# Optimization experiments

Hardware: AMD Instinct MI355X
Metric: run time of the kernel (lower is better)

Reference implementation:

```python
import jax, jax.numpy as jnp
import numpy as np

B, C, H, W = 16, 3, 224, 224
P = 16
D = 768
DFF = 3072
NH = 12
HD = D // NH
L = 12
NCLS = 1000
S = (H // P) * (W // P) + 1  # 197
EPS = 1e-6


def layernorm(x, g, b):
    mu = jnp.mean(x, axis=-1, keepdims=True)
    var = jnp.mean(jnp.square(x - mu), axis=-1, keepdims=True)
    return (x - mu) * jax.lax.rsqrt(var + EPS) * g + b


def setup_inputs() -> dict:
    key = jax.random.key(0)
    ks = jax.random.split(key, 24)
    s = 0.02
    inp = {
        "x": jax.random.normal(ks[0], (B, C, H, W), jnp.float32),
        "Wconv": jax.random.normal(ks[1], (D, C, P, P), jnp.float32) * s,
        "bconv": jnp.zeros((D,), jnp.float32),
        "cls_emb": jax.random.normal(ks[2], (1, 1, D), jnp.float32) * s,
        "pos_emb": jax.random.normal(ks[3], (1, S, D), jnp.float32) * s,
        "Wq": jax.random.normal(ks[4], (L, D, D), jnp.float32) * s,
        "bq": jnp.zeros((L, D), jnp.float32),
        "Wk": jax.random.normal(ks[5], (L, D, D), jnp.float32) * s,
        "bk": jnp.zeros((L, D), jnp.float32),
        "Wv": jax.random.normal(ks[6], (L, D, D), jnp.float32) * s,
        "bv": jnp.zeros((L, D), jnp.float32),
        "Wo": jax.random.normal(ks[7], (L, D, D), jnp.float32) * s,
        "bo": jnp.zeros((L, D), jnp.float32),
        "ln1_g": jnp.ones((L, D), jnp.float32),
        "ln1_b": jnp.zeros((L, D), jnp.float32),
        "Wff1": jax.random.normal(ks[8], (L, DFF, D), jnp.float32) * s,
        "bff1": jnp.zeros((L, DFF), jnp.float32),
        "Wff2": jax.random.normal(ks[9], (L, D, DFF), jnp.float32) * s,
        "bff2": jnp.zeros((L, D), jnp.float32),
        "ln2_g": jnp.ones((L, D), jnp.float32),
        "ln2_b": jnp.zeros((L, D), jnp.float32),
        "lnf_g": jnp.ones((D,), jnp.float32),
        "lnf_b": jnp.zeros((D,), jnp.float32),
        "Whead": jax.random.normal(ks[10], (NCLS, D), jnp.float32) * s,
        "bhead": jnp.zeros((NCLS,), jnp.float32),
    }
    return inp


def reference(x, Wconv, bconv, cls_emb, pos_emb, Wq, bq, Wk, bk, Wv, bv, Wo, bo,
              ln1_g, ln1_b, Wff1, bff1, Wff2, bff2, ln2_g, ln2_b,
              lnf_g, lnf_b, Whead, bhead):
    b = x.shape[0]
    # conv patch embedding: [B, D, H/P, W/P]
    h = jax.lax.conv_general_dilated(x, Wconv, window_strides=(P, P), padding='VALID',
                                     dimension_numbers=('NCHW', 'OIHW', 'NCHW'))
    h = h + bconv[None, :, None, None]
    h = h.reshape(b, D, -1).transpose(0, 2, 1)  # [B, 196, D]
    h = jnp.concatenate([jnp.broadcast_to(cls_emb, (b, 1, D)), h], axis=1)  # [B, S, D]
    h = h + pos_emb

    scale = 1.0 / np.sqrt(HD)
    all_scores = []
    for i in range(L):
        # pre-norm MHA
        n = layernorm(h, ln1_g[i], ln1_b[i])
        q = (jnp.einsum('bsd,ed->bse', n, Wq[i]) + bq[i]).reshape(b, S, NH, HD).transpose(0, 2, 1, 3)
        k = (jnp.einsum('bsd,ed->bse', n, Wk[i]) + bk[i]).reshape(b, S, NH, HD).transpose(0, 2, 1, 3)
        v = (jnp.einsum('bsd,ed->bse', n, Wv[i]) + bv[i]).reshape(b, S, NH, HD).transpose(0, 2, 1, 3)
        scores = jax.nn.softmax(jnp.einsum('bhqd,bhkd->bhqk', q, k) * scale, axis=-1)
        attn = jnp.einsum('bhqk,bhkd->bhqd', scores, v).transpose(0, 2, 1, 3).reshape(b, S, D)
        h = h + jnp.einsum('bsd,ed->bse', attn, Wo[i]) + bo[i]
        # pre-norm FFN (exact GELU, matching torch F.gelu default)
        n = layernorm(h, ln2_g[i], ln2_b[i])
        ff = jax.nn.gelu(jnp.einsum('bsd,fd->bsf', n, Wff1[i]) + bff1[i], approximate=False)
        h = h + jnp.einsum('bsf,df->bsd', ff, Wff2[i]) + bff2[i]
        all_scores.append(scores)

    cls = layernorm(h, lnf_g, lnf_b)[:, 0]  # [B, D]
    logits = cls @ Whead.T + bhead  # [B, NCLS]
    return logits, jnp.stack(all_scores)  # scores: [L, B, NH, S, S]
```

## Files before the change

### kernel.cpp

```cpp
#include <hip/hip_runtime.h>
#include <hip/hip_bf16.h>

#define L_   12
#define B_   16
#define S_   197
#define D_   768
#define DFF_ 3072
#define NH_  12
#define HD_  64
#define NCLS_ 1000
#define MROWS (B_*S_)
#define MPAD  3200
#define SPAD  224
#define BH_   (B_*NH_)
#define SP_   232

typedef short s16x8 __attribute__((ext_vector_type(8)));
typedef float f32x4 __attribute__((ext_vector_type(4)));
typedef unsigned short u16x4 __attribute__((ext_vector_type(4)));

__device__ inline unsigned short f2b(float f) {
  unsigned u = __builtin_bit_cast(unsigned, f);
  u += 0x7fffu + ((u >> 16) & 1u);
  return (unsigned short)(u >> 16);
}

__device__ inline f32x4 mfma16(s16x8 a, s16x8 b, f32x4 c) {
  return __builtin_amdgcn_mfma_f32_16x16x32_bf16(a, b, c, 0, 0, 0);
}

__device__ inline void gload16(const void* g, void* l) {
  __builtin_amdgcn_global_load_lds(
      (const __attribute__((address_space(1))) unsigned int*)g,
      (__attribute__((address_space(3))) unsigned int*)l,
      16, 0, 0);
}

__global__ __launch_bounds__(256) void cvt_bf16(const float* __restrict__ in,
                                                unsigned short* __restrict__ out, long n4) {
  long i = (long)blockIdx.x * 256 + threadIdx.x;
  long stride = (long)gridDim.x * 256;
  for (; i < n4; i += stride) {
    f32x4 v = ((const f32x4*)in)[i];
    u16x4 o = { f2b(v[0]), f2b(v[1]), f2b(v[2]), f2b(v[3]) };
    ((u16x4*)out)[i] = o;
  }
}

__global__ __launch_bounds__(256) void cvt_qkv(const float* __restrict__ Wq,
                                               const float* __restrict__ Wk,
                                               const float* __restrict__ Wv,
                                               unsigned short* __restrict__ dst) {
  const int l = blockIdx.z, sel = blockIdx.y;
  const float* src = (sel == 0 ? Wq : (sel == 1 ? Wk : Wv)) + (size_t)l * D_ * D_;
  unsigned short* d = dst + ((size_t)l * 3 + sel) * D_ * D_;
  int i4 = blockIdx.x * 256 + threadIdx.x;
  f32x4 v = ((const f32x4*)src)[i4];
  u16x4 o = { f2b(v[0]), f2b(v[1]), f2b(v[2]), f2b(v[3]) };
  ((u16x4*)d)[i4] = o;
}

__global__ __launch_bounds__(256) void cvt_bias_qkv(const float* __restrict__ bq,
                                                    const float* __restrict__ bk,
                                                    const float* __restrict__ bv,
                                                    float* __restrict__ dst) {
  int i = blockIdx.x * 256 + threadIdx.x;
  int l = i / 2304, r = i - l * 2304;
  int sel = r / 768, c = r - sel * 768;
  dst[i] = (sel == 0 ? bq : (sel == 1 ? bk : bv))[l * 768 + c];
}

__global__ __launch_bounds__(256) void im2col(const float* __restrict__ x,
                                              unsigned short* __restrict__ Xp) {
  int idx = blockIdx.x * 256 + threadIdx.x;
  if (idx >= 3136 * 768) return;
  int m = idx / 768, kk = idx - m * 768;
  int b = m / 196, p = m - b * 196;
  int ph = p / 14, pw = p - ph * 14;
  int c = kk >> 8, rr = kk & 255;
  int i = rr >> 4, j = rr & 15;
  float v = x[(((size_t)b * 3 + c) * 224 + ph * 16 + i) * 224 + pw * 16 + j];
  Xp[idx] = f2b(v);
}

__global__ __launch_bounds__(256) void cls_init(float* __restrict__ h,
                                                const float* __restrict__ cls,
                                                const float* __restrict__ pos) {
  int idx = blockIdx.x * 256 + threadIdx.x;
  if (idx >= B_ * D_) return;
  int b = idx / D_, d = idx - b * D_;
  h[(size_t)(b * S_) * D_ + d] = cls[d] + pos[d];
}

__global__ __launch_bounds__(256) void zero_vtpad(unsigned short* __restrict__ vT) {
  int idx = blockIdx.x * 256 + threadIdx.x;
  const int n = B_ * D_ * (SPAD - S_);
  if (idx >= n) return;
  int be = idx / (SPAD - S_), s = idx - be * (SPAD - S_);
  vT[(size_t)be * SPAD + S_ + s] = 0;
}

template<int MODE, int KSPLIT>
__global__ __launch_bounds__(256) void gemm_bt(const unsigned short* __restrict__ A,
                                               const unsigned short* __restrict__ W,
                                               const float* __restrict__ bias,
                                               const float* __restrict__ pos,
                                               float* __restrict__ Cf,
                                               unsigned short* __restrict__ Cb,
                                               unsigned short* __restrict__ Cb2,
                                               unsigned short* __restrict__ Cb3,
                                               int M, int N, int K, int lda) {
  __shared__ unsigned short As[2][128 * 32];
  __shared__ unsigned short Bs[2][128 * 32];
  const int t = threadIdx.x;
  const int lane = t & 63;
  const int w = t >> 6;
  const int wr = (w >> 1) << 6;
  const int wc = (w & 1) << 6;
  const size_t tileM = (size_t)blockIdx.x * 128;
  const int tileN = blockIdx.y * 128;
  const int kbeg = (KSPLIT > 1) ? blockIdx.z * (K / KSPLIT) : 0;
  const int nsteps = (K / KSPLIT) / 32;
  const int rrow = lane & 15;
  const int kk8 = (lane >> 4) << 3;
  const int r0 = t >> 2;
  const int c0 = (t & 3) << 3;
  const unsigned short* ga0 = A + (tileM + r0) * (size_t)lda + kbeg + c0;
  const unsigned short* ga1 = ga0 + (size_t)64 * lda;
  const unsigned short* gb0 = W + ((size_t)tileN + r0) * K + kbeg + c0;
  const unsigned short* gb1 = gb0 + (size_t)64 * K;
  auto stage = [&](int buf, int kof) {
    gload16(ga0 + kof, As[buf] + w * 512);
    gload16(ga1 + kof, As[buf] + 2048 + w * 512);
    gload16(gb0 + kof, Bs[buf] + w * 512);
    gload16(gb1 + kof, Bs[buf] + 2048 + w * 512);
  };
  f32x4 acc[4][4] = {};
  stage(0, 0);
  __syncthreads();
  int cur = 0;
  for (int ks = 0; ks < nsteps; ++ks) {
    if (ks + 1 < nsteps) stage(cur ^ 1, (ks + 1) * 32);
    s16x8 af[4], bfr[4];
#pragma unroll
    for (int i = 0; i < 4; ++i)
      af[i] = *(const s16x8*)(As[cur] + (wr + i * 16 + rrow) * 32 + kk8);
#pragma unroll
    for (int i = 0; i < 4; ++i)
      bfr[i] = *(const s16x8*)(Bs[cur] + (wc + i * 16 + rrow) * 32 + kk8);
#pragma unroll
    for (int mi = 0; mi < 4; ++mi)
#pragma unroll
      for (int ni = 0; ni < 4; ++ni)
        acc[mi][ni] = mfma16(af[mi], bfr[ni], acc[mi][ni]);
    if (ks + 1 < nsteps) { __syncthreads(); cur ^= 1; }
  }
  const int rg = lane >> 4;
#pragma unroll
  for (int mi = 0; mi < 4; ++mi) {
#pragma unroll
    for (int ni = 0; ni < 4; ++ni) {
#pragma unroll
      for (int r = 0; r < 4; ++r) {
        int row = (int)tileM + wr + mi * 16 + rg * 4 + r;
        int col = tileN + wc + ni * 16 + rrow;
        if (row < M) {
          float v = acc[mi][ni][r];
          if (MODE == 2) {
            v += bias[col];
            float g = 0.5f * v * (1.0f + erff(v * 0.70710678118654752f));
            Cb[(size_t)row * N + col] = f2b(g);
          } else if (MODE == 3) {
            int bb = row / 196, pp = row - bb * 196;
            v += bias[col] + pos[(size_t)(1 + pp) * D_ + col];
            Cf[((size_t)(bb * 197 + 1 + pp)) * D_ + col] = v;
          } else if (MODE == 5) {
            v += bias[col];
            unsigned short bv = f2b(v);
            if (col < 768) {
              Cb[(size_t)row * 768 + col] = bv;
            } else if (col < 1536) {
              Cb2[(size_t)row * 768 + (col - 768)] = bv;
            } else {
              int bb = row / 197, ss = row - bb * 197;
              Cb3[((size_t)bb * D_ + (col - 1536)) * SPAD + ss] = bv;
            }
          } else if (MODE == 6) {
            Cf[((size_t)blockIdx.z * MROWS + row) * N + col] = v;
          }
        }
      }
    }
  }
}

template<int NS, bool CLS>
__global__ __launch_bounds__(256) void reduce_ln(const float* __restrict__ P,
                                                 const float* __restrict__ bias,
                                                 float* __restrict__ h,
                                                 const float* __restrict__ g,
                                                 const float* __restrict__ bb,
                                                 unsigned short* __restrict__ nbuf,
                                                 const float* __restrict__ g2,
                                                 const float* __restrict__ b2,
                                                 float* __restrict__ cls_out) {
  const int r = blockIdx.x;
  const int t = threadIdx.x;
  float* hr = h + (size_t)r * D_;
  float v[3];
#pragma unroll
  for (int j = 0; j < 3; ++j) {
    const int c = t + j * 256;
    float a = hr[c] + bias[c];
#pragma unroll
    for (int z = 0; z < NS; ++z)
      a += P[((size_t)z * MROWS + r) * D_ + c];
    v[j] = a;
  }
  float s = v[0] + v[1] + v[2];
  float s2 = v[0] * v[0] + v[1] * v[1] + v[2] * v[2];
  __shared__ float rs_[4], rs2_[4];
  const int lane = t & 63, w = t >> 6;
#pragma unroll
  for (int m = 32; m; m >>= 1) { s += __shfl_xor(s, m); s2 += __shfl_xor(s2, m); }
  if (lane == 0) { rs_[w] = s; rs2_[w] = s2; }
  __syncthreads();
  s = rs_[0] + rs_[1] + rs_[2] + rs_[3];
  s2 = rs2_[0] + rs2_[1] + rs2_[2] + rs2_[3];
  const float mu = s * (1.0f / 768.0f);
  const float var = s2 * (1.0f / 768.0f) - mu * mu;
  const float rstd = rsqrtf(var + 1e-6f);
  if (!CLS) {
    unsigned short* o = nbuf + (size_t)r * D_;
#pragma unroll
    for (int j = 0; j < 3; ++j) {
      const int c = t + j * 256;
      hr[c] = v[j];
      o[c] = f2b((v[j] - mu) * rstd * g[c] + bb[c]);
    }
  } else {
    if (r % S_ == 0) {
      float* o = cls_out + (size_t)(r / S_) * D_;
#pragma unroll
      for (int j = 0; j < 3; ++j) {
        const int c = t + j * 256;
        o[c] = (v[j] - mu) * rstd * g2[c] + b2[c];
      }
    }
  }
}

__global__ __launch_bounds__(256) void ln_rows_bf16(const float* __restrict__ x,
                                                    const float* __restrict__ g,
                                                    const float* __restrict__ bb,
                                                    unsigned short* __restrict__ out) {
  const int row = blockIdx.x;
  const float* xr = x + (size_t)row * D_;
  const int t = threadIdx.x;
  float v0 = xr[t], v1 = xr[t + 256], v2 = xr[t + 512];
  float s = v0 + v1 + v2;
  float s2 = v0 * v0 + v1 * v1 + v2 * v2;
  __shared__ float rs_[4], rs2_[4];
  const int lane = t & 63, w = t >> 6;
#pragma unroll
  for (int m = 32; m; m >>= 1) { s += __shfl_xor(s, m); s2 += __shfl_xor(s2, m); }
  if (lane == 0) { rs_[w] = s; rs2_[w] = s2; }
  __syncthreads();
  s = rs_[0] + rs_[1] + rs_[2] + rs_[3];
  s2 = rs2_[0] + rs2_[1] + rs2_[2] + rs2_[3];
  const float mu = s * (1.0f / 768.0f);
  const float var = s2 * (1.0f / 768.0f) - mu * mu;
  const float rstd = rsqrtf(var + 1e-6f);
  unsigned short* o = out + (size_t)row * D_;
  o[t]       = f2b((v0 - mu) * rstd * g[t]       + bb[t]);
  o[t + 256] = f2b((v1 - mu) * rstd * g[t + 256] + bb[t + 256]);
  o[t + 512] = f2b((v2 - mu) * rstd * g[t + 512] + bb[t + 512]);
}

__global__ __launch_bounds__(64) void attn_fused(const unsigned short* __restrict__ q,
                                                 const unsigned short* __restrict__ k,
                                                 const unsigned short* __restrict__ vT,
                                                 float* __restrict__ sout,
                                                 unsigned short* __restrict__ attn) {
  __shared__ unsigned short sP[16 * SP_];
  const int bh = blockIdx.x;
  const int b = bh / NH_, h = bh % NH_;
  const int strip = blockIdx.y;
  const int lane = threadIdx.x;
  const int rrow = lane & 15;
  const int kk8 = (lane >> 4) << 3;
  const int rg = lane >> 4;
  const unsigned short* qb = q + ((size_t)b * S_) * D_ + h * HD_;
  const unsigned short* kb = k + ((size_t)b * S_) * D_ + h * HD_;
  f32x4 acc[13] = {};
#pragma unroll
  for (int ks = 0; ks < 2; ++ks) {
    s16x8 af = *(const s16x8*)(qb + (size_t)(strip * 16 + rrow) * D_ + ks * 32 + kk8);
#pragma unroll
    for (int nf = 0; nf < 13; ++nf) {
      s16x8 bfr = *(const s16x8*)(kb + (size_t)(nf * 16 + rrow) * D_ + ks * 32 + kk8);
      acc[nf] = mfma16(af, bfr, acc[nf]);
    }
  }
#pragma unroll
  for (int r = 0; r < 4; ++r) {
    const int lr = rg * 4 + r;
    const int row = strip * 16 + lr;
    float mx = -1e30f;
#pragma unroll
    for (int nf = 0; nf < 13; ++nf) {
      int col = nf * 16 + rrow;
      float v = acc[nf][r] * 0.125f;
      if (col < S_) mx = fmaxf(mx, v);
    }
#pragma unroll
    for (int m = 1; m < 16; m <<= 1) mx = fmaxf(mx, __shfl_xor(mx, m));
    float e[13], sum = 0.f;
#pragma unroll
    for (int nf = 0; nf < 13; ++nf) {
      int col = nf * 16 + rrow;
      e[nf] = (col < S_) ? expf(acc[nf][r] * 0.125f - mx) : 0.f;
      sum += e[nf];
    }
#pragma unroll
    for (int m = 1; m < 16; m <<= 1) sum += __shfl_xor(sum, m);
    const float inv = 1.0f / sum;
    float* so = sout + ((size_t)bh * S_ + row) * S_;
#pragma unroll
    for (int nf = 0; nf < 13; ++nf) {
      int col = nf * 16 + rrow;
      float p = e[nf] * inv;
      if (row < S_ && col < S_) so[col] = p;
      sP[lr * SP_ + col] = f2b((col < S_) ? p : 0.f);
    }
  }
#pragma unroll
  for (int j = 0; j < 6; ++j) {
    int idx = lane + j * 64;
    int pr = idx / 24, pc = idx - pr * 24;
    sP[pr * SP_ + 208 + pc] = 0;
  }
  const unsigned short* Vb = vT + ((size_t)b * D_ + h * HD_) * SPAD;
  f32x4 oacc[4] = {};
#pragma unroll
  for (int ks = 0; ks < 7; ++ks) {
    s16x8 af = *(const s16x8*)(sP + rrow * SP_ + ks * 32 + kk8);
#pragma unroll
    for (int nf = 0; nf < 4; ++nf) {
      s16x8 bfr = *(const s16x8*)(Vb + (size_t)(nf * 16 + rrow) * SPAD + ks * 32 + kk8);
      oacc[nf] = mfma16(af, bfr, oacc[nf]);
    }
  }
#pragma unroll
  for (int r = 0; r < 4; ++r) {
    int row = strip * 16 + rg * 4 + r;
    if (row < S_) {
#pragma unroll
      for (int nf = 0; nf < 4; ++nf) {
        int col = h * HD_ + nf * 16 + rrow;
        attn[(size_t)(b * S_ + row) * D_ + col] = f2b(oacc[nf][r]);
      }
    }
  }
}

__global__ __launch_bounds__(256) void head_kernel(const float* __restrict__ cls_ln,
                                                   const float* __restrict__ Wh,
                                                   const float* __restrict__ bh_,
                                                   float* __restrict__ out) {
  int gw = (blockIdx.x * 256 + threadIdx.x) >> 6;
  int lane = threadIdx.x & 63;
  if (gw >= B_ * NCLS_) return;
  int b = gw / NCLS_, c = gw - b * NCLS_;
  const float* x = cls_ln + (size_t)b * D_;
  const float* wr = Wh + (size_t)c * D_;
  float s = 0.f;
  for (int d = lane; d < D_; d += 64) s += x[d] * wr[d];
#pragma unroll
  for (int m = 32; m; m >>= 1) s += __shfl_xor(s, m);
  if (lane == 0) out[(size_t)b * NCLS_ + c] = s + bh_[c];
}

extern "C" void kernel_launch(void* const* d_in, const int* in_sizes, int n_in,
                              void* d_out, int out_size, void* d_ws, size_t ws_size,
                              hipStream_t stream) {
  const float* x     = (const float*)d_in[0];
  const float* Wconv = (const float*)d_in[1];
  const float* bconv = (const float*)d_in[2];
  const float* cls_e = (const float*)d_in[3];
  const float* pos_e = (const float*)d_in[4];
  const float* Wq    = (const float*)d_in[5];
  const float* bq    = (const float*)d_in[6];
  const float* Wk    = (const float*)d_in[7];
  const float* bk    = (const float*)d_in[8];
  const float* Wv    = (const float*)d_in[9];
  const float* bv    = (const float*)d_in[10];
  const float* Wo    = (const float*)d_in[11];
  const float* bo    = (const float*)d_in[12];
  const float* ln1g  = (const float*)d_in[13];
  const float* ln1b  = (const float*)d_in[14];
  const float* Wff1  = (const float*)d_in[15];
  const float* bff1  = (const float*)d_in[16];
  const float* Wff2  = (const float*)d_in[17];
  const float* bff2  = (const float*)d_in[18];
  const float* ln2g  = (const float*)d_in[19];
  const float* ln2b  = (const float*)d_in[20];
  const float* lnfg  = (const float*)d_in[21];
  const float* lnfb  = (const float*)d_in[22];
  const float* Whead = (const float*)d_in[23];
  const float* bhead = (const float*)d_in[24];

  char* base = (char*)d_ws;
  size_t off = 0;
  auto alloc = [&](size_t bytes) {
    void* p = base + off;
    off = (off + bytes + 255) & ~(size_t)255;
    return p;
  };
  unsigned short* Wqkv_b = (unsigned short*)alloc((size_t)L_ * 3 * D_ * D_ * 2);
  unsigned short* Wo_b   = (unsigned short*)alloc((size_t)L_ * D_ * D_ * 2);
  unsigned short* Wff1_b = (unsigned short*)alloc((size_t)L_ * DFF_ * D_ * 2);
  unsigned short* Wff2_b = (unsigned short*)alloc((size_t)L_ * D_ * DFF_ * 2);
  unsigned short* Wconv_b= (unsigned short*)alloc((size_t)D_ * D_ * 2);
  float*          bqkv   = (float*)alloc((size_t)L_ * 2304 * 4);
  float*          h      = (float*)alloc((size_t)MPAD * D_ * 4);
  unsigned short* nbuf   = (unsigned short*)alloc((size_t)MPAD * D_ * 2);
  unsigned short* qbuf   = (unsigned short*)alloc((size_t)MPAD * D_ * 2);
  unsigned short* kbuf   = (unsigned short*)alloc((size_t)MPAD * D_ * 2);
  unsigned short* vT     = (unsigned short*)alloc((size_t)B_ * D_ * SPAD * 2);
  unsigned short* attn   = (unsigned short*)alloc((size_t)MPAD * D_ * 2);
  unsigned short* ff     = (unsigned short*)alloc((size_t)MPAD * DFF_ * 2);
  unsigned short* Xp     = (unsigned short*)alloc((size_t)MPAD * D_ * 2);
  float*          Po     = (float*)alloc((size_t)2 * MROWS * D_ * 4);
  float*          Pf     = (float*)alloc((size_t)4 * MROWS * D_ * 4);
  float*          cls_ln = (float*)alloc((size_t)B_ * D_ * 4);
  (void)ws_size; (void)in_sizes; (void)n_in; (void)out_size;

  float* out_f = (float*)d_out;
  float* scores_base = out_f + (size_t)B_ * NCLS_;

  cvt_qkv<<<dim3(576, 3, L_), 256, 0, stream>>>(Wq, Wk, Wv, Wqkv_b);
  cvt_bf16<<<2048, 256, 0, stream>>>(Wo,   Wo_b,   (long)L_ * D_ * D_ / 4);
  cvt_bf16<<<2048, 256, 0, stream>>>(Wff1, Wff1_b, (long)L_ * DFF_ * D_ / 4);
  cvt_bf16<<<2048, 256, 0, stream>>>(Wff2, Wff2_b, (long)L_ * D_ * DFF_ / 4);
  cvt_bf16<<<576, 256, 0, stream>>>(Wconv, Wconv_b, (long)D_ * D_ / 4);
  cvt_bias_qkv<<<(L_ * 2304) / 256, 256, 0, stream>>>(bq, bk, bv, bqkv);

  im2col<<<(3136 * 768) / 256, 256, 0, stream>>>(x, Xp);
  gemm_bt<3, 1><<<dim3(25, 6), 256, 0, stream>>>(Xp, Wconv_b, bconv, pos_e, h,
                                                 nullptr, nullptr, nullptr, 3136, D_, D_, D_);
  cls_init<<<(B_ * D_ + 255) / 256, 256, 0, stream>>>(h, cls_e, pos_e);
  zero_vtpad<<<(B_ * D_ * (SPAD - S_) + 255) / 256, 256, 0, stream>>>(vT);
  ln_rows_bf16<<<MROWS, 256, 0, stream>>>(h, ln1g, ln1b, nbuf);

  for (int l = 0; l < L_; ++l) {
    const unsigned short* wqkv = Wqkv_b + (size_t)l * 3 * D_ * D_;
    const unsigned short* wo = Wo_b + (size_t)l * D_ * D_;
    const unsigned short* w1 = Wff1_b + (size_t)l * DFF_ * D_;
    const unsigned short* w2 = Wff2_b + (size_t)l * D_ * DFF_;
    float* sc = scores_base + (size_t)l * BH_ * S_ * S_;

    gemm_bt<5, 1><<<dim3(25, 18), 256, 0, stream>>>(nbuf, wqkv, bqkv + l * 2304, nullptr,
                                                    nullptr, qbuf, kbuf, vT, MROWS, 2304, D_, D_);
    attn_fused<<<dim3(BH_, 13), 64, 0, stream>>>(qbuf, kbuf, vT, sc, attn);
    gemm_bt<6, 2><<<dim3(25, 6, 2), 256, 0, stream>>>(attn, wo, nullptr, nullptr, Po,
                                                      nullptr, nullptr, nullptr, MROWS, D_, D_, D_);
    reduce_ln<2, false><<<MROWS, 256, 0, stream>>>(Po, bo + l * D_, h,
                                                   ln2g + l * D_, ln2b + l * D_, nbuf,
                                                   nullptr, nullptr, nullptr);
    gemm_bt<2, 1><<<dim3(25, 24), 256, 0, stream>>>(nbuf, w1, bff1 + l * DFF_, nullptr,
                                                    nullptr, ff, nullptr, nullptr, MROWS, DFF_, D_, D_);
    gemm_bt<6, 4><<<dim3(25, 6, 4), 256, 0, stream>>>(ff, w2, nullptr, nullptr, Pf,
                                                      nullptr, nullptr, nullptr, MROWS, D_, DFF_, DFF_);
    if (l < L_ - 1) {
      reduce_ln<4, false><<<MROWS, 256, 0, stream>>>(Pf, bff2 + l * D_, h,
                                                     ln1g + (l + 1) * D_, ln1b + (l + 1) * D_, nbuf,
                                                     nullptr, nullptr, nullptr);
    } else {
      reduce_ln<4, true><<<MROWS, 256, 0, stream>>>(Pf, bff2 + l * D_, h,
                                                    nullptr, nullptr, nullptr,
                                                    lnfg, lnfb, cls_ln);
    }
  }

  head_kernel<<<(B_ * NCLS_ * 64) / 256, 256, 0, stream>>>(cls_ln, Whead, bhead, out_f);
}
```

Baseline: 2.376 ms.

## Deepen GEMM K-tile to 64 with swizzled LDS, XCD remap, trim final LN

```diff
diff --git a/kernel.cpp b/kernel.cpp
--- a/kernel.cpp
+++ b/kernel.cpp
@@ -101,58 +101,74 @@
 }
 
 template<int MODE, int KSPLIT>
-__global__ __launch_bounds__(256) void gemm_bt(const unsigned short* __restrict__ A,
-                                               const unsigned short* __restrict__ W,
-                                               const float* __restrict__ bias,
-                                               const float* __restrict__ pos,
-                                               float* __restrict__ Cf,
-                                               unsigned short* __restrict__ Cb,
-                                               unsigned short* __restrict__ Cb2,
-                                               unsigned short* __restrict__ Cb3,
-                                               int M, int N, int K, int lda) {
-  __shared__ unsigned short As[2][128 * 32];
-  __shared__ unsigned short Bs[2][128 * 32];
+__global__ __launch_bounds__(256, 2) void gemm_bt(const unsigned short* __restrict__ A,
+                                                  const unsigned short* __restrict__ W,
+                                                  const float* __restrict__ bias,
+                                                  const float* __restrict__ pos,
+                                                  float* __restrict__ Cf,
+                                                  unsigned short* __restrict__ Cb,
+                                                  unsigned short* __restrict__ Cb2,
+                                                  unsigned short* __restrict__ Cb3,
+                                                  int M, int N, int K, int lda) {
+  __shared__ unsigned short As[2][128 * 64];
+  __shared__ unsigned short Bs[2][128 * 64];
   const int t = threadIdx.x;
   const int lane = t & 63;
   const int w = t >> 6;
+  const int gx = gridDim.x, gy = gridDim.y;
+  const int nwg = gx * gy * gridDim.z;
+  int orig = (blockIdx.z * gy + blockIdx.y) * gx + blockIdx.x;
+  int q8 = nwg >> 3, r8 = nwg & 7;
+  int xcd = orig & 7, idx8 = orig >> 3;
+  int wgid = (xcd < r8 ? xcd * (q8 + 1) : r8 * (q8 + 1) + (xcd - r8) * q8) + idx8;
+  int tz = wgid / (gx * gy);
+  int rem = wgid - tz * gx * gy;
+  int tx = rem / gy;
+  int ty = rem - tx * gy;
+  const size_t tileM = (size_t)tx * 128;
+  const int tileN = ty * 128;
+  const int kbeg = (KSPLIT > 1) ? tz * (K / KSPLIT) : 0;
+  const int nsteps = (K / KSPLIT) / 64;
+  const int l8 = lane >> 3;
+  const int u  = lane & 7;
+  const int su = u ^ l8;
+  const unsigned short* gaB = A + kbeg + su * 8 + (size_t)(tileM + (size_t)w * 32 + l8) * lda;
+  const unsigned short* gbB = W + kbeg + su * 8 + (size_t)(tileN + (size_t)w * 32 + l8) * K;
+  auto stage = [&](int buf, int kof) {
+#pragma unroll
+    for (int j = 0; j < 4; ++j)
+      gload16(gaB + (size_t)(j * 8) * lda + kof, As[buf] + (w * 4 + j) * 512);
+#pragma unroll
+    for (int j = 0; j < 4; ++j)
+      gload16(gbB + (size_t)(j * 8) * K + kof, Bs[buf] + (w * 4 + j) * 512);
+  };
   const int wr = (w >> 1) << 6;
   const int wc = (w & 1) << 6;
-  const size_t tileM = (size_t)blockIdx.x * 128;
-  const int tileN = blockIdx.y * 128;
-  const int kbeg = (KSPLIT > 1) ? blockIdx.z * (K / KSPLIT) : 0;
-  const int nsteps = (K / KSPLIT) / 32;
   const int rrow = lane & 15;
-  const int kk8 = (lane >> 4) << 3;
-  const int r0 = t >> 2;
-  const int c0 = (t & 3) << 3;
-  const unsigned short* ga0 = A + (tileM + r0) * (size_t)lda + kbeg + c0;
-  const unsigned short* ga1 = ga0 + (size_t)64 * lda;
-  const unsigned short* gb0 = W + ((size_t)tileN + r0) * K + kbeg + c0;
-  const unsigned short* gb1 = gb0 + (size_t)64 * K;
-  auto stage = [&](int buf, int kof) {
-    gload16(ga0 + kof, As[buf] + w * 512);
-    gload16(ga1 + kof, As[buf] + 2048 + w * 512);
-    gload16(gb0 + kof, Bs[buf] + w * 512);
-    gload16(gb1 + kof, Bs[buf] + 2048 + w * 512);
-  };
+  const int hi = lane >> 4;
+  const int r7 = lane & 7;
   f32x4 acc[4][4] = {};
   stage(0, 0);
   __syncthreads();
   int cur = 0;
   for (int ks = 0; ks < nsteps; ++ks) {
-    if (ks + 1 < nsteps) stage(cur ^ 1, (ks + 1) * 32);
-    s16x8 af[4], bfr[4];
-#pragma unroll
-    for (int i = 0; i < 4; ++i)
-      af[i] = *(const s16x8*)(As[cur] + (wr + i * 16 + rrow) * 32 + kk8);
-#pragma unroll
-    for (int i = 0; i < 4; ++i)
-      bfr[i] = *(const s16x8*)(Bs[cur] + (wc + i * 16 + rrow) * 32 + kk8);
-#pragma unroll
-    for (int mi = 0; mi < 4; ++mi)
-#pragma unroll
-      for (int ni = 0; ni < 4; ++ni)
-        acc[mi][ni] = mfma16(af[mi], bfr[ni], acc[mi][ni]);
+    if (ks + 1 < nsteps) stage(cur ^ 1, (ks + 1) * 64);
+#pragma unroll
+    for (int kh = 0; kh < 2; ++kh) {
+      const int uk = ((kh * 4 + hi) ^ r7) * 8;
+      s16x8 af[4], bfr[4];
+#pragma unroll
+      for (int i = 0; i < 4; ++i)
+        af[i] = *(const s16x8*)(As[cur] + (wr + i * 16 + rrow) * 64 + uk);
+#pragma unroll
+      for (int i = 0; i < 4; ++i)
+        bfr[i] = *(const s16x8*)(Bs[cur] + (wc + i * 16 + rrow) * 64 + uk);
+#pragma unroll
+      for (int mi = 0; mi < 4; ++mi)
+#pragma unroll
+        for (int ni = 0; ni < 4; ++ni)
+          acc[mi][ni] = mfma16(af[mi], bfr[ni], acc[mi][ni]);
+    }
     if (ks + 1 < nsteps) { __syncthreads(); cur ^= 1; }
   }
   const int rg = lane >> 4;
@@ -186,7 +202,7 @@
               Cb3[((size_t)bb * D_ + (col - 1536)) * SPAD + ss] = bv;
             }
           } else if (MODE == 6) {
-            Cf[((size_t)blockIdx.z * MROWS + row) * N + col] = v;
+            Cf[((size_t)tz * MROWS + row) * N + col] = v;
           }
         }
       }
@@ -204,7 +220,7 @@
                                                  const float* __restrict__ g2,
                                                  const float* __restrict__ b2,
                                                  float* __restrict__ cls_out) {
-  const int r = blockIdx.x;
+  const int r = CLS ? blockIdx.x * S_ : blockIdx.x;
   const int t = threadIdx.x;
   float* hr = h + (size_t)r * D_;
   float v[3];
@@ -239,13 +255,11 @@
       o[c] = f2b((v[j] - mu) * rstd * g[c] + bb[c]);
     }
   } else {
-    if (r % S_ == 0) {
-      float* o = cls_out + (size_t)(r / S_) * D_;
-#pragma unroll
-      for (int j = 0; j < 3; ++j) {
-        const int c = t + j * 256;
-        o[c] = (v[j] - mu) * rstd * g2[c] + b2[c];
-      }
+    float* o = cls_out + (size_t)blockIdx.x * D_;
+#pragma unroll
+    for (int j = 0; j < 3; ++j) {
+      const int c = t + j * 256;
+      o[c] = (v[j] - mu) * rstd * g2[c] + b2[c];
     }
   }
 }
@@ -477,9 +491,9 @@
                                                      ln1g + (l + 1) * D_, ln1b + (l + 1) * D_, nbuf,
                                                      nullptr, nullptr, nullptr);
     } else {
-      reduce_ln<4, true><<<MROWS, 256, 0, stream>>>(Pf, bff2 + l * D_, h,
-                                                    nullptr, nullptr, nullptr,
-                                                    lnfg, lnfb, cls_ln);
+      reduce_ln<4, true><<<B_, 256, 0, stream>>>(Pf, bff2 + l * D_, h,
+                                                 nullptr, nullptr, nullptr,
+                                                 lnfg, lnfb, cls_ln);
     }
   }
 
```

New measurement: 2.526 ms. 6.3% more time.
